# Kernel optimization log

Measured on AMD Instinct MI355X. Metric: run time of the kernel, lower is better.

## Reference

```python
import jax, jax.numpy as jnp
import numpy as np

TEMPERATURE = 1.0

def setup_inputs() -> dict:
    key = jax.random.key(0)
    k1, k2 = jax.random.split(key)
    z1 = jax.random.normal(k1, (8, 256, 2048), dtype=jnp.float32)
    z2 = jax.random.normal(k2, (8, 256, 2048), dtype=jnp.float32)
    return {"z1": z1, "z2": z2}

def reference(z1, z2):
    # logits[b, n, m] = sum_s z1[b, s, n] * z2[b, s, m], scaled by temperature
    logits = jnp.einsum('bsn,bsm->bnm', z1, z2) / TEMPERATURE
    # torch F.cross_entropy on (b, C=n, m) with labels[b, m] = m:
    # softmax over axis 1 (n), then gather the diagonal n == m.
    logp = jax.nn.log_softmax(logits, axis=1)        # (b, n, m)
    diag = jnp.diagonal(logp, axis1=1, axis2=2)      # (b, m) = logp[b, m, m]
    return -jnp.mean(diag)
```

## Files before the change

kernel.cpp:

```cpp
#include <hip/hip_runtime.h>
#include <hip/hip_bf16.h>


#define NN 2048
#define SK 256
#define LDST 264
#define LOG2E 1.4426950408889634f
#define LN2   0.6931471805599453f
#define COFF  96.0f

typedef __attribute__((ext_vector_type(8))) short short8;
typedef __attribute__((ext_vector_type(16))) float f32x16;

__device__ __forceinline__ unsigned short f2bf(float f) {
    __hip_bfloat16 h = __float2bfloat16(f);
    unsigned short u; __builtin_memcpy(&u, &h, 2); return u;
}

__device__ __forceinline__ float exp2g(float x) {
#if __has_builtin(__builtin_amdgcn_exp2f)
    return __builtin_amdgcn_exp2f(x);
#else
    return exp2f(x);
#endif
}

__device__ __forceinline__ float log2g(float x) {
#if __has_builtin(__builtin_amdgcn_logf)
    return __builtin_amdgcn_logf(x);
#else
    return log2f(x);
#endif
}

__global__ __launch_bounds__(512, 2) void gemm_lse_kernel(
    const float* __restrict__ z1, const float* __restrict__ z2,
    float* __restrict__ ws_sum, float* __restrict__ ws_diag)
{
    __shared__ unsigned short ldsA[2][64 * LDST];

    const int bid  = blockIdx.x;
    const int b    = bid & 7;
    const int tile = bid >> 3;
    const int mb   = tile & 7;
    const int ns   = tile >> 3;
    const int tid  = threadIdx.x;
    const int lane = tid & 63;
    const int w    = tid >> 6;
    const int wm   = w >> 1;
    const int wn   = w & 1;
    const int col  = lane & 31;
    const int kg   = lane >> 5;

    const int m0      = mb * 256 + wm * 64;
    const int mcol0   = m0 + col;
    const int mcol1   = m0 + 32 + col;
    const int n_start = ns * 512;

    const float* z1b = z1 + (size_t)b * SK * NN;
    const float* z2b = z2 + (size_t)b * SK * NN;

    float apf[4][8];
    auto load_A = [&](int t) {
        const int nbase = n_start + 64 * t;
        #pragma unroll
        for (int r = 0; r < 4; ++r) {
            const int sg = 8 * r + w;
            const float* p = z1b + (size_t)(sg * 8) * NN + nbase + lane;
            #pragma unroll
            for (int j = 0; j < 8; ++j) apf[r][j] = p[(size_t)j * NN];
        }
    };
    auto store_A = [&](unsigned short* buf) {
        #pragma unroll
        for (int r = 0; r < 4; ++r) {
            const int sg = 8 * r + w;
            short8 pk;
            #pragma unroll
            for (int j = 0; j < 8; ++j) pk[j] = (short)f2bf(apf[r][j]);
            *(short8*)(buf + lane * LDST + sg * 8) = pk;
        }
    };

    load_A(0);
    store_A(ldsA[0]);
    load_A(1);

    short8 bf0[16], bf1[16];
    #pragma unroll
    for (int ks = 0; ks < 16; ++ks) {
        short8 p0, p1;
        #pragma unroll
        for (int j = 0; j < 8; ++j) {
            const int s = ks * 16 + kg * 8 + j;
            p0[j] = (short)f2bf(z2b[s * NN + mcol0] * LOG2E);
            p1[j] = (short)f2bf(z2b[s * NN + mcol1] * LOG2E);
        }
        bf0[ks] = p0; bf1[ks] = p1;
    }

    float srun0 = 0.0f, srun1 = 0.0f;

    __syncthreads();

    for (int t = 0; t < 8; ++t) {
        const unsigned short* abase = ldsA[t & 1] + (32 * wn + col) * LDST + kg * 8;

        f32x16 acc0, acc1;
        #pragma unroll
        for (int r = 0; r < 16; ++r) { acc0[r] = -COFF; acc1[r] = -COFF; }

        #pragma unroll
        for (int ks = 0; ks < 16; ++ks) {
            short8 af = *(const short8*)(abase + ks * 16);
            acc0 = __builtin_amdgcn_mfma_f32_32x32x16_bf16(af, bf0[ks], acc0, 0, 0, 0);
            acc1 = __builtin_amdgcn_mfma_f32_32x32x16_bf16(af, bf1[ks], acc1, 0, 0, 0);
        }

        if (t < 7) store_A(ldsA[(t + 1) & 1]);
        if (t < 6) load_A(t + 2);

        const int nsub = n_start + 64 * t + 32 * wn;
        if (nsub == m0) {
            #pragma unroll
            for (int r = 0; r < 16; ++r) {
                const int row = (r & 3) + 8 * (r >> 2) + 4 * kg;
                if (row == col) ws_diag[b * NN + mcol0] = acc0[r];
            }
        }
        if (nsub == m0 + 32) {
            #pragma unroll
            for (int r = 0; r < 16; ++r) {
                const int row = (r & 3) + 8 * (r >> 2) + 4 * kg;
                if (row == col) ws_diag[b * NN + mcol1] = acc1[r];
            }
        }

        {
            float e0 = 0, e1 = 0, e2 = 0, e3 = 0;
            #pragma unroll
            for (int r = 0; r < 16; r += 4) {
                e0 += exp2g(acc0[r]);     e1 += exp2g(acc0[r + 1]);
                e2 += exp2g(acc0[r + 2]); e3 += exp2g(acc0[r + 3]);
            }
            srun0 += (e0 + e1) + (e2 + e3);
        }
        {
            float e0 = 0, e1 = 0, e2 = 0, e3 = 0;
            #pragma unroll
            for (int r = 0; r < 16; r += 4) {
                e0 += exp2g(acc1[r]);     e1 += exp2g(acc1[r + 1]);
                e2 += exp2g(acc1[r + 2]); e3 += exp2g(acc1[r + 3]);
            }
            srun1 += (e0 + e1) + (e2 + e3);
        }

        __syncthreads();
    }

    srun0 += __shfl_xor(srun0, 32);
    srun1 += __shfl_xor(srun1, 32);
    if (kg == 0) {
        const int slot = ns * 2 + wn;
        ws_sum[(b * 8 + slot) * NN + mcol0] = srun0;
        ws_sum[(b * 8 + slot) * NN + mcol1] = srun1;
    }
}

__global__ __launch_bounds__(256) void merge_kernel(
    const float* __restrict__ ws_sum, const float* __restrict__ ws_diag,
    float* __restrict__ partial)
{
    const int gid = blockIdx.x * 256 + threadIdx.x;
    const int b = gid >> 11, m = gid & (NN - 1);

    float S = 0.0f;
    #pragma unroll
    for (int slot = 0; slot < 8; ++slot)
        S += ws_sum[(b * 8 + slot) * NN + m];
    float c = log2g(S) - ws_diag[gid];

    #pragma unroll
    for (int d = 1; d < 64; d <<= 1) c += __shfl_xor(c, d);
    __shared__ float red[4];
    if ((threadIdx.x & 63) == 0) red[threadIdx.x >> 6] = c;
    __syncthreads();
    if (threadIdx.x == 0)
        partial[blockIdx.x] = red[0] + red[1] + red[2] + red[3];
}

__global__ void final_kernel(const float* __restrict__ partial, float* __restrict__ out)
{
    float v = partial[threadIdx.x];
    #pragma unroll
    for (int d = 1; d < 64; d <<= 1) v += __shfl_xor(v, d);
    if (threadIdx.x == 0) out[0] = v * (LN2 / 16384.0f);
}

extern "C" void kernel_launch(void* const* d_in, const int* in_sizes, int n_in,
                              void* d_out, int out_size, void* d_ws, size_t ws_size,
                              hipStream_t stream)
{
    const float* z1 = (const float*)d_in[0];
    const float* z2 = (const float*)d_in[1];
    float* ws  = (float*)d_ws;
    float* out = (float*)d_out;

    float* ws_sum  = ws;
    float* ws_diag = ws + 131072;
    float* ws_part = ws + 147456;

    gemm_lse_kernel<<<dim3(256), dim3(512), 0, stream>>>(z1, z2, ws_sum, ws_diag);
    merge_kernel<<<dim3(64), dim3(256), 0, stream>>>(ws_sum, ws_diag, ws_part);
    final_kernel<<<dim3(1), dim3(64), 0, stream>>>(ws_part, out);
}
```

Baseline: 32.20 us.

## Stage B operand through LDS with coalesced loads instead of strided per-lane gathers

The B fragments (z2 columns) were previously loaded by each lane directly from global memory with a stride of one row per element, giving poorly coalesced accesses. They are now loaded with the same coalesced, transposing pattern used for A, converted to bf16 in LDS in double-buffered 64-column chunks, and each warp-row group reads its fragments from LDS. The A prefetch is chained onto the end of this pipeline, and the main loop is unrolled by 2. This adds several barriers and LDS round-trips to the prologue.

```diff
diff --git a/kernel.cpp b/kernel.cpp
--- a/kernel.cpp
+++ b/kernel.cpp
@@ -37,7 +37,7 @@
     const float* __restrict__ z1, const float* __restrict__ z2,
     float* __restrict__ ws_sum, float* __restrict__ ws_diag)
 {
-    __shared__ unsigned short ldsA[2][64 * LDST];
+    __shared__ unsigned short lds[2][64 * LDST];
 
     const int bid  = blockIdx.x;
     const int b    = bid & 7;
@@ -52,21 +52,19 @@
     const int col  = lane & 31;
     const int kg   = lane >> 5;
 
-    const int m0      = mb * 256 + wm * 64;
-    const int mcol0   = m0 + col;
-    const int mcol1   = m0 + 32 + col;
-    const int n_start = ns * 512;
+    const int m0    = mb * 256 + wm * 64;
+    const int mcol0 = m0 + col;
+    const int mcol1 = m0 + 32 + col;
 
     const float* z1b = z1 + (size_t)b * SK * NN;
     const float* z2b = z2 + (size_t)b * SK * NN;
 
     float apf[4][8];
-    auto load_A = [&](int t) {
-        const int nbase = n_start + 64 * t;
+    auto load_T = [&](const float* src, int cbase) {
         #pragma unroll
         for (int r = 0; r < 4; ++r) {
             const int sg = 8 * r + w;
-            const float* p = z1b + (size_t)(sg * 8) * NN + nbase + lane;
+            const float* p = src + (size_t)(sg * 8) * NN + cbase + lane;
             #pragma unroll
             for (int j = 0; j < 8; ++j) apf[r][j] = p[(size_t)j * NN];
         }
@@ -81,30 +79,47 @@
             *(short8*)(buf + lane * LDST + sg * 8) = pk;
         }
     };
-
-    load_A(0);
-    store_A(ldsA[0]);
-    load_A(1);
+    auto store_B = [&](unsigned short* buf) {
+        #pragma unroll
+        for (int r = 0; r < 4; ++r) {
+            const int sg = 8 * r + w;
+            short8 pk;
+            #pragma unroll
+            for (int j = 0; j < 8; ++j) pk[j] = (short)f2bf(apf[r][j] * LOG2E);
+            *(short8*)(buf + lane * LDST + sg * 8) = pk;
+        }
+    };
 
     short8 bf0[16], bf1[16];
-    #pragma unroll
-    for (int ks = 0; ks < 16; ++ks) {
-        short8 p0, p1;
-        #pragma unroll
-        for (int j = 0; j < 8; ++j) {
-            const int s = ks * 16 + kg * 8 + j;
-            p0[j] = (short)f2bf(z2b[s * NN + mcol0] * LOG2E);
-            p1[j] = (short)f2bf(z2b[s * NN + mcol1] * LOG2E);
-        }
-        bf0[ks] = p0; bf1[ks] = p1;
+
+    load_T(z2b, mb * 256);
+    store_B(lds[0]);
+    load_T(z2b, mb * 256 + 64);
+    __syncthreads();
+
+    #pragma unroll
+    for (int j = 0; j < 4; ++j) {
+        if (wm == j) {
+            const unsigned short* b0 = lds[j & 1] + col * LDST + kg * 8;
+            const unsigned short* b1 = lds[j & 1] + (32 + col) * LDST + kg * 8;
+            #pragma unroll
+            for (int ks = 0; ks < 16; ++ks) {
+                bf0[ks] = *(const short8*)(b0 + ks * 16);
+                bf1[ks] = *(const short8*)(b1 + ks * 16);
+            }
+        }
+        if (j < 3) store_B(lds[(j + 1) & 1]);
+        else       store_A(lds[0]);
+        if (j < 2) load_T(z2b, mb * 256 + (j + 2) * 64);
+        else       load_T(z1b, ns * 512 + (j - 2) * 64);
+        __syncthreads();
     }
 
     float srun0 = 0.0f, srun1 = 0.0f;
 
-    __syncthreads();
-
+    #pragma unroll 2
     for (int t = 0; t < 8; ++t) {
-        const unsigned short* abase = ldsA[t & 1] + (32 * wn + col) * LDST + kg * 8;
+        const unsigned short* abase = lds[t & 1] + (32 * wn + col) * LDST + kg * 8;
 
         f32x16 acc0, acc1;
         #pragma unroll
@@ -117,10 +132,10 @@
             acc1 = __builtin_amdgcn_mfma_f32_32x32x16_bf16(af, bf1[ks], acc1, 0, 0, 0);
         }
 
-        if (t < 7) store_A(ldsA[(t + 1) & 1]);
-        if (t < 6) load_A(t + 2);
-
-        const int nsub = n_start + 64 * t + 32 * wn;
+        if (t < 7) store_A(lds[(t + 1) & 1]);
+        if (t < 6) load_T(z1b, ns * 512 + (t + 2) * 64);
+
+        const int nsub = ns * 512 + 64 * t + 32 * wn;
         if (nsub == m0) {
             #pragma unroll
             for (int r = 0; r < 16; ++r) {
```

Result: slower. 44.12 us (+37.0%).

## Software-pipeline exp2 reduction of previous tile under current tile's MFMAs

Applied to the files above, without the earlier changes.

Fully unrolls the 8-tile loop with ping-pong accumulator sets so the exp2 sums of the previous tile's logits are interleaved with the MFMA chain of the current tile. The goal is to hide transcendental/VALU work behind matrix-core latency instead of serializing it after each tile. This doubles live accumulator registers (64 extra VGPRs/AGPRs), which may pressure the 2-waves-per-SIMD launch bound and cause spills.

```diff
diff --git a/kernel.cpp b/kernel.cpp
--- a/kernel.cpp
+++ b/kernel.cpp
@@ -37,7 +37,7 @@
     const float* __restrict__ z1, const float* __restrict__ z2,
     float* __restrict__ ws_sum, float* __restrict__ ws_diag)
 {
-    __shared__ unsigned short ldsA[2][64 * LDST];
+    __shared__ unsigned short lds[2][64 * LDST];
 
     const int bid  = blockIdx.x;
     const int b    = bid & 7;
@@ -83,7 +83,7 @@
     };
 
     load_A(0);
-    store_A(ldsA[0]);
+    store_A(lds[0]);
     load_A(1);
 
     short8 bf0[16], bf1[16];
@@ -100,62 +100,78 @@
     }
 
     float srun0 = 0.0f, srun1 = 0.0f;
+    f32x16 accE0, accE1, accO0, accO1;
 
     __syncthreads();
 
-    for (int t = 0; t < 8; ++t) {
-        const unsigned short* abase = ldsA[t & 1] + (32 * wn + col) * LDST + kg * 8;
-
-        f32x16 acc0, acc1;
-        #pragma unroll
-        for (int r = 0; r < 16; ++r) { acc0[r] = -COFF; acc1[r] = -COFF; }
-
-        #pragma unroll
-        for (int ks = 0; ks < 16; ++ks) {
-            short8 af = *(const short8*)(abase + ks * 16);
-            acc0 = __builtin_amdgcn_mfma_f32_32x32x16_bf16(af, bf0[ks], acc0, 0, 0, 0);
-            acc1 = __builtin_amdgcn_mfma_f32_32x32x16_bf16(af, bf1[ks], acc1, 0, 0, 0);
-        }
-
-        if (t < 7) store_A(ldsA[(t + 1) & 1]);
-        if (t < 6) load_A(t + 2);
-
-        const int nsub = n_start + 64 * t + 32 * wn;
-        if (nsub == m0) {
-            #pragma unroll
-            for (int r = 0; r < 16; ++r) {
-                const int row = (r & 3) + 8 * (r >> 2) + 4 * kg;
-                if (row == col) ws_diag[b * NN + mcol0] = acc0[r];
-            }
-        }
-        if (nsub == m0 + 32) {
-            #pragma unroll
-            for (int r = 0; r < 16; ++r) {
-                const int row = (r & 3) + 8 * (r >> 2) + 4 * kg;
-                if (row == col) ws_diag[b * NN + mcol1] = acc1[r];
-            }
-        }
-
-        {
-            float e0 = 0, e1 = 0, e2 = 0, e3 = 0;
-            #pragma unroll
-            for (int r = 0; r < 16; r += 4) {
-                e0 += exp2g(acc0[r]);     e1 += exp2g(acc0[r + 1]);
-                e2 += exp2g(acc0[r + 2]); e3 += exp2g(acc0[r + 3]);
-            }
-            srun0 += (e0 + e1) + (e2 + e3);
-        }
-        {
-            float e0 = 0, e1 = 0, e2 = 0, e3 = 0;
-            #pragma unroll
-            for (int r = 0; r < 16; r += 4) {
-                e0 += exp2g(acc1[r]);     e1 += exp2g(acc1[r + 1]);
-                e2 += exp2g(acc1[r + 2]); e3 += exp2g(acc1[r + 3]);
-            }
-            srun1 += (e0 + e1) + (e2 + e3);
-        }
-
-        __syncthreads();
+#define TILE_BODY(T, C0, C1, P0, P1, DOP)                                           \
+    {                                                                               \
+        const unsigned short* abase = lds[(T) & 1] + (32 * wn + col) * LDST + kg * 8; \
+        _Pragma("unroll")                                                           \
+        for (int r = 0; r < 16; ++r) { C0[r] = -COFF; C1[r] = -COFF; }              \
+        float f0 = 0, f1 = 0, f2 = 0, f3 = 0, g0 = 0, g1 = 0, g2 = 0, g3 = 0;       \
+        _Pragma("unroll")                                                           \
+        for (int ks = 0; ks < 16; ++ks) {                                           \
+            short8 af = *(const short8*)(abase + ks * 16);                          \
+            C0 = __builtin_amdgcn_mfma_f32_32x32x16_bf16(af, bf0[ks], C0, 0, 0, 0); \
+            C1 = __builtin_amdgcn_mfma_f32_32x32x16_bf16(af, bf1[ks], C1, 0, 0, 0); \
+            if ((DOP) && (ks & 1)) {                                                \
+                const int c = ks >> 1;                                              \
+                if (c < 4) {                                                        \
+                    f0 += exp2g(P0[(4 * c + 0) & 15]);                              \
+                    f1 += exp2g(P0[(4 * c + 1) & 15]);                              \
+                    f2 += exp2g(P0[(4 * c + 2) & 15]);                              \
+                    f3 += exp2g(P0[(4 * c + 3) & 15]);                              \
+                } else {                                                            \
+                    g0 += exp2g(P1[(4 * c + 0) & 15]);                              \
+                    g1 += exp2g(P1[(4 * c + 1) & 15]);                              \
+                    g2 += exp2g(P1[(4 * c + 2) & 15]);                              \
+                    g3 += exp2g(P1[(4 * c + 3) & 15]);                              \
+                }                                                                   \
+            }                                                                       \
+        }                                                                           \
+        if (DOP) { srun0 += (f0 + f1) + (f2 + f3); srun1 += (g0 + g1) + (g2 + g3); } \
+        if ((T) < 7) store_A(lds[((T) + 1) & 1]);                                   \
+        if ((T) < 6) load_A((T) + 2);                                               \
+        const int nsub = n_start + 64 * (T) + 32 * wn;                              \
+        if (nsub == m0) {                                                           \
+            _Pragma("unroll")                                                       \
+            for (int r = 0; r < 16; ++r) {                                          \
+                const int row = (r & 3) + 8 * (r >> 2) + 4 * kg;                    \
+                if (row == col) ws_diag[b * NN + mcol0] = C0[r];                    \
+            }                                                                       \
+        }                                                                           \
+        if (nsub == m0 + 32) {                                                      \
+            _Pragma("unroll")                                                       \
+            for (int r = 0; r < 16; ++r) {                                          \
+                const int row = (r & 3) + 8 * (r >> 2) + 4 * kg;                    \
+                if (row == col) ws_diag[b * NN + mcol1] = C1[r];                    \
+            }                                                                       \
+        }                                                                           \
+        __syncthreads();                                                            \
+    }
+
+    TILE_BODY(0, accE0, accE1, accO0, accO1, false)
+    TILE_BODY(1, accO0, accO1, accE0, accE1, true)
+    TILE_BODY(2, accE0, accE1, accO0, accO1, true)
+    TILE_BODY(3, accO0, accO1, accE0, accE1, true)
+    TILE_BODY(4, accE0, accE1, accO0, accO1, true)
+    TILE_BODY(5, accO0, accO1, accE0, accE1, true)
+    TILE_BODY(6, accE0, accE1, accO0, accO1, true)
+    TILE_BODY(7, accO0, accO1, accE0, accE1, true)
+#undef TILE_BODY
+
+    {
+        float f0 = 0, f1 = 0, f2 = 0, f3 = 0, g0 = 0, g1 = 0, g2 = 0, g3 = 0;
+        #pragma unroll
+        for (int r = 0; r < 16; r += 4) {
+            f0 += exp2g(accO0[r]);     f1 += exp2g(accO0[r + 1]);
+            f2 += exp2g(accO0[r + 2]); f3 += exp2g(accO0[r + 3]);
+            g0 += exp2g(accO1[r]);     g1 += exp2g(accO1[r + 1]);
+            g2 += exp2g(accO1[r + 2]); g3 += exp2g(accO1[r + 3]);
+        }
+        srun0 += (f0 + f1) + (f2 + f3);
+        srun1 += (g0 + g1) + (g2 + g3);
     }
 
     srun0 += __shfl_xor(srun0, 32);
```

Result: slower. 118.4 us (+267.9%).

## Retile GEMM-LSE blocks to 512 m-columns by 256 n-rows with 32-row A tiles

Applied to the files above, without the earlier changes.

Changes the block tiling so each block covers 512 m-columns (8 waves × 64) and 256 n-rows. It streams 32-row A tiles through a smaller LDS double buffer, where every wave shares the same A tile instead of splitting by wn. A-tile loading is restructured so each thread loads 16 contiguous-k values, and the B register prefetch is split around the first A load to overlap the two. The occupancy hint of 2 blocks is dropped. The intent is to raise reuse of each A tile across more waves and cut LDS footprint, at the cost of more loop iterations per unit of work and possible register-pressure changes.

```diff
diff --git a/kernel.cpp b/kernel.cpp
--- a/kernel.cpp
+++ b/kernel.cpp
@@ -33,78 +33,73 @@
 #endif
 }
 
-__global__ __launch_bounds__(512, 2) void gemm_lse_kernel(
+__global__ __launch_bounds__(512) void gemm_lse_kernel(
     const float* __restrict__ z1, const float* __restrict__ z2,
     float* __restrict__ ws_sum, float* __restrict__ ws_diag)
 {
-    __shared__ unsigned short ldsA[2][64 * LDST];
+    __shared__ unsigned short lds[2][32 * LDST];
 
     const int bid  = blockIdx.x;
     const int b    = bid & 7;
     const int tile = bid >> 3;
-    const int mb   = tile & 7;
-    const int ns   = tile >> 3;
+    const int mb   = tile & 3;
+    const int ns   = tile >> 2;
     const int tid  = threadIdx.x;
     const int lane = tid & 63;
     const int w    = tid >> 6;
-    const int wm   = w >> 1;
-    const int wn   = w & 1;
     const int col  = lane & 31;
     const int kg   = lane >> 5;
 
-    const int m0      = mb * 256 + wm * 64;
+    const int m0      = mb * 512 + w * 64;
     const int mcol0   = m0 + col;
     const int mcol1   = m0 + 32 + col;
-    const int n_start = ns * 512;
+    const int n_start = ns * 256;
 
     const float* z1b = z1 + (size_t)b * SK * NN;
     const float* z2b = z2 + (size_t)b * SK * NN;
 
-    float apf[4][8];
+    const int kc  = (w << 1) | kg;
+    const int row = col;
+    float apf[16];
     auto load_A = [&](int t) {
-        const int nbase = n_start + 64 * t;
-        #pragma unroll
-        for (int r = 0; r < 4; ++r) {
-            const int sg = 8 * r + w;
-            const float* p = z1b + (size_t)(sg * 8) * NN + nbase + lane;
-            #pragma unroll
-            for (int j = 0; j < 8; ++j) apf[r][j] = p[(size_t)j * NN];
-        }
+        const float* p = z1b + (size_t)(kc * 16) * NN + (n_start + 32 * t + row);
+        #pragma unroll
+        for (int j = 0; j < 16; ++j) apf[j] = p[(size_t)j * NN];
     };
     auto store_A = [&](unsigned short* buf) {
-        #pragma unroll
-        for (int r = 0; r < 4; ++r) {
-            const int sg = 8 * r + w;
-            short8 pk;
-            #pragma unroll
-            for (int j = 0; j < 8; ++j) pk[j] = (short)f2bf(apf[r][j]);
-            *(short8*)(buf + lane * LDST + sg * 8) = pk;
-        }
+        short8 pk0, pk1;
+        #pragma unroll
+        for (int j = 0; j < 8; ++j) { pk0[j] = (short)f2bf(apf[j]); pk1[j] = (short)f2bf(apf[j + 8]); }
+        *(short8*)(buf + row * LDST + kc * 16)     = pk0;
+        *(short8*)(buf + row * LDST + kc * 16 + 8) = pk1;
     };
 
-    load_A(0);
-    store_A(ldsA[0]);
-    load_A(1);
-
     short8 bf0[16], bf1[16];
-    #pragma unroll
-    for (int ks = 0; ks < 16; ++ks) {
+    auto loadB = [&](int ks) {
         short8 p0, p1;
         #pragma unroll
         for (int j = 0; j < 8; ++j) {
             const int s = ks * 16 + kg * 8 + j;
-            p0[j] = (short)f2bf(z2b[s * NN + mcol0] * LOG2E);
-            p1[j] = (short)f2bf(z2b[s * NN + mcol1] * LOG2E);
+            p0[j] = (short)f2bf(z2b[(size_t)s * NN + mcol0] * LOG2E);
+            p1[j] = (short)f2bf(z2b[(size_t)s * NN + mcol1] * LOG2E);
         }
         bf0[ks] = p0; bf1[ks] = p1;
-    }
+    };
+
+    #pragma unroll
+    for (int ks = 0; ks < 8; ++ks) loadB(ks);
+    load_A(0);
+    store_A(lds[0]);
+    load_A(1);
+    #pragma unroll
+    for (int ks = 8; ks < 16; ++ks) loadB(ks);
 
     float srun0 = 0.0f, srun1 = 0.0f;
 
     __syncthreads();
 
     for (int t = 0; t < 8; ++t) {
-        const unsigned short* abase = ldsA[t & 1] + (32 * wn + col) * LDST + kg * 8;
+        const unsigned short* abase = lds[t & 1] + col * LDST + kg * 8;
 
         f32x16 acc0, acc1;
         #pragma unroll
@@ -117,22 +112,22 @@
             acc1 = __builtin_amdgcn_mfma_f32_32x32x16_bf16(af, bf1[ks], acc1, 0, 0, 0);
         }
 
-        if (t < 7) store_A(ldsA[(t + 1) & 1]);
+        if (t < 7) store_A(lds[(t + 1) & 1]);
         if (t < 6) load_A(t + 2);
 
-        const int nsub = n_start + 64 * t + 32 * wn;
+        const int nsub = n_start + 32 * t;
         if (nsub == m0) {
             #pragma unroll
             for (int r = 0; r < 16; ++r) {
-                const int row = (r & 3) + 8 * (r >> 2) + 4 * kg;
-                if (row == col) ws_diag[b * NN + mcol0] = acc0[r];
+                const int rw = (r & 3) + 8 * (r >> 2) + 4 * kg;
+                if (rw == col) ws_diag[b * NN + mcol0] = acc0[r];
             }
         }
         if (nsub == m0 + 32) {
             #pragma unroll
             for (int r = 0; r < 16; ++r) {
-                const int row = (r & 3) + 8 * (r >> 2) + 4 * kg;
-                if (row == col) ws_diag[b * NN + mcol1] = acc1[r];
+                const int rw = (r & 3) + 8 * (r >> 2) + 4 * kg;
+                if (rw == col) ws_diag[b * NN + mcol1] = acc1[r];
             }
         }
 
@@ -161,9 +156,8 @@
     srun0 += __shfl_xor(srun0, 32);
     srun1 += __shfl_xor(srun1, 32);
     if (kg == 0) {
-        const int slot = ns * 2 + wn;
-        ws_sum[(b * 8 + slot) * NN + mcol0] = srun0;
-        ws_sum[(b * 8 + slot) * NN + mcol1] = srun1;
+        ws_sum[(b * 8 + ns) * NN + mcol0] = srun0;
+        ws_sum[(b * 8 + ns) * NN + mcol1] = srun1;
     }
 }
 
```

New measurement: 30.13 us. -6.4%, faster.
